# Performance work log

Measured on AMD Instinct MI355X. Metric: run time of the kernel, lower is better.

Reference implementation:

```python
import jax, jax.numpy as jnp
import numpy as np

N_NODES = 50000
N_EDGES = 800000
HIDDEN = 128
BN_EPS = 1e-5
LEAKY_SLOPE = 0.01


def setup_inputs() -> dict:
    key = jax.random.key(0)
    ks = jax.random.split(key, 8)
    x = jax.random.normal(ks[0], (N_NODES, HIDDEN), dtype=jnp.float32)
    edge_index = jax.random.randint(ks[1], (2, N_EDGES), 0, N_NODES, dtype=jnp.int64)
    # stacked per-layer params (4 SAGEConv layers, all 128->128)
    sc = 1.0 / np.sqrt(HIDDEN)
    Wl = jax.random.normal(ks[2], (4, HIDDEN, HIDDEN), dtype=jnp.float32) * sc
    bl = jax.random.normal(ks[3], (4, HIDDEN), dtype=jnp.float32) * sc
    Wr = jax.random.normal(ks[4], (4, HIDDEN, HIDDEN), dtype=jnp.float32) * sc
    gamma = jnp.ones((4, HIDDEN), dtype=jnp.float32)
    beta = jnp.zeros((4, HIDDEN), dtype=jnp.float32)
    return {"x": x, "edge_index": edge_index, "Wl": Wl, "bl": bl,
            "Wr": Wr, "gamma": gamma, "beta": beta}


def _sage_mean_agg(x, src, dst, n):
    # gather source features per edge, scatter-mean onto destination nodes
    msg = x[src]                                                  # [E, F]
    agg = jax.ops.segment_sum(msg, dst, num_segments=n)           # [N, F]
    cnt = jax.ops.segment_sum(jnp.ones_like(dst, dtype=x.dtype), dst, num_segments=n)
    return agg / jnp.maximum(cnt, 1.0)[:, None]


def _bn_train(x, g, b):
    mu = jnp.mean(x, axis=0)
    var = jnp.mean((x - mu) ** 2, axis=0)  # biased variance (PyTorch BN normalization)
    return (x - mu) * jax.lax.rsqrt(var + BN_EPS) * g + b


def reference(x, edge_index, Wl, bl, Wr, gamma, beta):
    src, dst = edge_index[0], edge_index[1]
    n = x.shape[0]
    h = x
    for i in range(4):
        agg = _sage_mean_agg(h, src, dst, n)
        h = agg @ Wl[i] + bl[i] + h @ Wr[i]          # SAGEConv: lin_l(mean_nbr) + lin_r(root)
        h = jnp.where(h >= 0, h, LEAKY_SLOPE * h)    # leaky_relu
        h = _bn_train(h, gamma[i], beta[i])
    # dropout: eval-mode identity (deterministic reference)
    return h
```

## Files before the change

kernel.cpp:

```cpp
#include <hip/hip_runtime.h>
#include <hip/hip_bf16.h>

#define N_NODES 50000
#define N_EDGES 800000
#define F 128
#define BN_EPS 1e-5f
#define SLOPE 0.01f
#define NB 782
#define CAP 64
#define NGRP 8
#define GSZ (N_NODES / NGRP)
#define QCAP 131072
#define ABLK 128
#define AITER ((N_EDGES + ABLK * 256 - 1) / (ABLK * 256))
#define SBLK 512

typedef __attribute__((ext_vector_type(8))) __bf16 bf16x8_t;
typedef __attribute__((ext_vector_type(8))) unsigned short u16x8_t;
typedef __attribute__((ext_vector_type(4))) float f32x4_t;

__device__ __forceinline__ unsigned short f2b(float f) {
    unsigned int u = __float_as_uint(f);
    unsigned int r = (u + 0x7fffu + ((u >> 16) & 1u)) >> 16;
    return (unsigned short)r;
}
__device__ __forceinline__ float b2f_lo(unsigned int v) { return __uint_as_float(v << 16); }
__device__ __forceinline__ float b2f_hi(unsigned int v) { return __uint_as_float(v & 0xffff0000u); }

__global__ __launch_bounds__(256) void bucket_kernel(const int* __restrict__ src,
                                                     const int* __restrict__ dst,
                                                     int* __restrict__ qtail,
                                                     unsigned int* __restrict__ qdata) {
    __shared__ unsigned int bins[4][NGRP][128];
    const int tid = threadIdx.x;
    const int lane = tid & 63;
    const int w = tid >> 6;
    int bc[NGRP];
#pragma unroll
    for (int k = 0; k < NGRP; ++k) bc[k] = 0;

    const int stride = ABLK * 256;
    for (int it = 0; it < AITER; ++it) {
        const int e = blockIdx.x * 256 + tid + it * stride;
        const bool valid = e < N_EDGES;
        int g = -1;
        unsigned int pack = 0;
        if (valid) {
            int d = __builtin_nontemporal_load(dst + e);
            int s = __builtin_nontemporal_load(src + e);
            g = d / GSZ;
            pack = ((unsigned int)d << 16) | (unsigned int)s;
        }
#pragma unroll
        for (int k = 0; k < NGRP; ++k) {
            unsigned long long mask = __ballot(g == k);
            int cnt = __popcll(mask);
            if (!cnt) continue;
            int cur = bc[k];
            if (cur + cnt > 128) {
                int qb = 0;
                if (lane == 0) qb = atomicAdd(&qtail[k * 16], cur);
                qb = __shfl(qb, 0);
                for (int j = lane; j < cur; j += 64)
                    qdata[(long)k * QCAP + qb + j] = bins[w][k][j];
                cur = 0;
            }
            if (g == k) {
                int rank = __popcll(mask & ((1ull << lane) - 1ull));
                bins[w][k][cur + rank] = pack;
            }
            bc[k] = cur + cnt;
        }
    }
#pragma unroll
    for (int k = 0; k < NGRP; ++k) {
        int cur = bc[k];
        if (cur) {
            int qb = 0;
            if (lane == 0) qb = atomicAdd(&qtail[k * 16], cur);
            qb = __shfl(qb, 0);
            for (int j = lane; j < cur; j += 64)
                qdata[(long)k * QCAP + qb + j] = bins[w][k][j];
        }
    }
}

__global__ void scatter_kernel(const unsigned int* __restrict__ qdata,
                               const int* __restrict__ qtail,
                               int* __restrict__ deg_pad,
                               unsigned short* __restrict__ csr) {
    const int g = blockIdx.x & 7;
    const int bg = blockIdx.x >> 3;
    const int n = qtail[g * 16];
    const unsigned int* q = qdata + (long)g * QCAP;
    for (int i = bg * 256 + threadIdx.x; i < n; i += (SBLK / 8) * 256) {
        unsigned int p = __builtin_nontemporal_load(q + i);
        int d = p >> 16;
        int s = p & 0xffff;
        int pos = atomicAdd(&deg_pad[d * 16], 1);
        if (pos < CAP) csr[d * CAP + pos] = (unsigned short)s;
    }
}


__global__ __launch_bounds__(256) void f2b_kernel(const float* __restrict__ in,
                                                  unsigned short* __restrict__ out) {
    long i = (long)blockIdx.x * blockDim.x + threadIdx.x;
    if (i >= (long)N_NODES * (F / 4)) return;
    float4 v = ((const float4*)in)[i];
    ushort4 o;
    o.x = f2b(v.x); o.y = f2b(v.y); o.z = f2b(v.z); o.w = f2b(v.w);
    ((ushort4*)out)[i] = o;
}

__global__ __launch_bounds__(256) void wprep_kernel(const float* __restrict__ Wl,
                                                    const float* __restrict__ Wr,
                                                    unsigned short* __restrict__ Wt) {
    int idx = blockIdx.x * blockDim.x + threadIdx.x;
    if (idx >= 4 * F * 256) return;
    int k = idx & 255;
    int n = (idx >> 8) & 127;
    int i = idx >> 15;
    float v = (k < F) ? Wl[((long)i * F + k) * F + n] : Wr[((long)i * F + (k - F)) * F + n];
    Wt[idx] = f2b(v);
}

__global__ void ident_kernel(float* __restrict__ scale, float* __restrict__ shift) {
    int j = threadIdx.x;
    if (j < F) { scale[j] = 1.f; shift[j] = 0.f; }
}


__global__ __launch_bounds__(256) void agg_kernel(const unsigned short* __restrict__ h,
                                                  const int* __restrict__ deg_pad,
                                                  const unsigned short* __restrict__ csr,
                                                  const float* __restrict__ scale,
                                                  const float* __restrict__ shift,
                                                  unsigned short* __restrict__ agg) {
    int node = (int)((blockIdx.x * (unsigned)blockDim.x + threadIdx.x) >> 6);
    int lane = threadIdx.x & 63;
    if (node >= N_NODES) return;
    const int d = deg_pad[node * 16];
    const int beg = node * CAP;
    const int end = beg + d;
    const unsigned short* hl = h + lane * 2;
    float ax = 0.f, ay = 0.f;
    for (int e = beg; e < end; e += 16) {
        int idx[16];
#pragma unroll
        for (int j = 0; j < 16; ++j) {
            int ee = e + j;
            idx[j] = (int)csr[(ee < end) ? ee : beg];
        }
        unsigned int v[16];
#pragma unroll
        for (int j = 0; j < 16; ++j)
            v[j] = *(const unsigned int*)(hl + (long)idx[j] * F);
#pragma unroll
        for (int j = 0; j < 16; ++j) {
            unsigned int m = (e + j < end) ? v[j] : 0u;
            ax += b2f_lo(m);
            ay += b2f_hi(m);
        }
    }
    if (d > 0) {
        const float inv = 1.0f / (float)d;
        const float2 sc = ((const float2*)scale)[lane];
        const float2 sh = ((const float2*)shift)[lane];
        ax = ax * inv * sc.x + sh.x;
        ay = ay * inv * sc.y + sh.y;
    } else {
        ax = 0.f; ay = 0.f;
    }
    unsigned int o = (unsigned int)f2b(ax) | ((unsigned int)f2b(ay) << 16);
    *(unsigned int*)(agg + (long)node * F + lane * 2) = o;
}

__device__ __forceinline__ u16x8_t affine8(u16x8_t av, const float* __restrict__ sc,
                                           const float* __restrict__ sh) {
    u16x8_t r;
#pragma unroll
    for (int j = 0; j < 8; ++j) {
        float v = __uint_as_float(((unsigned int)av[j]) << 16);
        v = v * sc[j] + sh[j];
        r[j] = f2b(v);
    }
    return r;
}

__global__ __launch_bounds__(256) void gemm_mfma(const unsigned short* __restrict__ aggb,
                                                 const unsigned short* __restrict__ hin,
                                                 const float* __restrict__ scale,
                                                 const float* __restrict__ shift,
                                                 const unsigned short* __restrict__ Wt,
                                                 const float* __restrict__ bl,
                                                 float* __restrict__ Pf,
                                                 unsigned short* __restrict__ Pb,
                                                 int write_bf16,
                                                 float* __restrict__ partial) {
    __shared__ __align__(16) char shraw[64 * 136 * 4];
    unsigned short* stage = (unsigned short*)shraw;
    unsigned short* ep16 = (unsigned short*)shraw;
    float* ep32 = (float*)shraw;
    __shared__ float lsum[4][F];
    __shared__ float lsq[4][F];

    const int tid = threadIdx.x;
    const int wave = tid >> 6, lane = tid & 63;
    const int m = lane & 15, q = lane >> 4;
    const int rbase = blockIdx.x * 64 + wave * 16;
    const int arow = rbase + m;
    const bool aval = arow < N_NODES;
    const unsigned short* ap = aggb + (long)arow * F + q * 8;
    const unsigned short* hp = hin + (long)arow * F + q * 8;

    u16x8_t areg[8];
#pragma unroll
    for (int j = 0; j < 8; ++j) areg[j] = (u16x8_t)0;
    if (aval) {
#pragma unroll
        for (int j = 0; j < 4; ++j) areg[j] = *(const u16x8_t*)(ap + j * 32);
#pragma unroll
        for (int j = 0; j < 4; ++j) {
            u16x8_t raw = *(const u16x8_t*)(hp + j * 32);
            const int base = j * 32 + q * 8;
            areg[4 + j] = affine8(raw, scale + base, shift + base);
        }
    }

    f32x4_t acc[8];
#pragma unroll
    for (int nt = 0; nt < 8; ++nt) acc[nt] = (f32x4_t){0.f, 0.f, 0.f, 0.f};

    for (int half = 0; half < 2; ++half) {
        if (half) __syncthreads();
#pragma unroll
        for (int f = 0; f < 8; ++f) {
            const int fid = f * 256 + tid;
            const int lf = fid & 63;
            const int ksf = (fid >> 6) & 3;
            const int ntf = fid >> 8;
            const int n = ntf * 16 + (lf & 15);
            const int k = half * 128 + ksf * 32 + (lf >> 4) * 8;
            *(u16x8_t*)(stage + fid * 8) = *(const u16x8_t*)(Wt + (long)n * 256 + k);
        }
        __syncthreads();
#pragma unroll
        for (int ks = 0; ks < 4; ++ks) {
            bf16x8_t af = __builtin_bit_cast(bf16x8_t, areg[half * 4 + ks]);
#pragma unroll
            for (int nt = 0; nt < 8; ++nt) {
                u16x8_t bv = *(const u16x8_t*)(stage + ((nt * 4 + ks) * 64 + lane) * 8);
                bf16x8_t bf = __builtin_bit_cast(bf16x8_t, bv);
                acc[nt] = __builtin_amdgcn_mfma_f32_16x16x32_bf16(af, bf, acc[nt], 0, 0, 0);
            }
        }
    }

    __syncthreads();

    float cs[8], cq[8];
#pragma unroll
    for (int nt = 0; nt < 8; ++nt) {
        cs[nt] = 0.f; cq[nt] = 0.f;
        const int c = nt * 16 + m;
        const float b = bl[c];
#pragma unroll
        for (int r = 0; r < 4; ++r) {
            const int rl = wave * 16 + q * 4 + r;
            float v = acc[nt][r] + b;
            v = (v >= 0.f) ? v : SLOPE * v;
            if (write_bf16) ep16[rl * 136 + c] = f2b(v);
            else            ep32[rl * 136 + c] = v;
            if (rbase + q * 4 + r < N_NODES) {
                cs[nt] += v;
                cq[nt] += v * v;
            }
        }
    }

    {
        const int rq = lane >> 4;
        const int cc = (lane & 15) * 8;
#pragma unroll
        for (int r2 = 0; r2 < 4; ++r2) {
            const int rl = wave * 16 + rq * 4 + r2;
            const int grow = blockIdx.x * 64 + rl;
            if (grow < N_NODES) {
                if (write_bf16) {
                    *(u16x8_t*)(Pb + (long)grow * F + cc) =
                        *(const u16x8_t*)(ep16 + rl * 136 + cc);
                } else {
                    *(f32x4_t*)(Pf + (long)grow * F + cc) =
                        *(const f32x4_t*)(ep32 + rl * 136 + cc);
                    *(f32x4_t*)(Pf + (long)grow * F + cc + 4) =
                        *(const f32x4_t*)(ep32 + rl * 136 + cc + 4);
                }
            }
        }
    }

#pragma unroll
    for (int nt = 0; nt < 8; ++nt) {
        cs[nt] += __shfl_xor(cs[nt], 16);
        cs[nt] += __shfl_xor(cs[nt], 32);
        cq[nt] += __shfl_xor(cq[nt], 16);
        cq[nt] += __shfl_xor(cq[nt], 32);
    }
    if (lane < 16) {
#pragma unroll
        for (int nt = 0; nt < 8; ++nt) {
            lsum[wave][nt * 16 + m] = cs[nt];
            lsq[wave][nt * 16 + m] = cq[nt];
        }
    }
    __syncthreads();
    if (tid < F) {
        float s = 0.f, s2 = 0.f;
#pragma unroll
        for (int w = 0; w < 4; ++w) {
            s += lsum[w][tid];
            s2 += lsq[w][tid];
        }
        partial[(long)blockIdx.x * 256 + tid] = s;
        partial[(long)blockIdx.x * 256 + 128 + tid] = s2;
    }
}

__global__ __launch_bounds__(256) void bn_reduce(const float* __restrict__ partial,
                                                 const float* __restrict__ gamma,
                                                 const float* __restrict__ beta,
                                                 float* __restrict__ scale,
                                                 float* __restrict__ shift) {
    const int j = blockIdx.x;
    const int t = threadIdx.x;
    const int lane = t & 63, wave = t >> 6;
    float s = 0.f, s2 = 0.f;
    for (int b = t; b < NB; b += 256) {
        s += partial[(long)b * 256 + j];
        s2 += partial[(long)b * 256 + 128 + j];
    }
#pragma unroll
    for (int off = 1; off < 64; off <<= 1) {
        s += __shfl_xor(s, off);
        s2 += __shfl_xor(s2, off);
    }
    __shared__ float ls[4], lq[4];
    if (lane == 0) { ls[wave] = s; lq[wave] = s2; }
    __syncthreads();
    if (t == 0) {
        float S = ls[0] + ls[1] + ls[2] + ls[3];
        float Q = lq[0] + lq[1] + lq[2] + lq[3];
        const float inv_n = 1.0f / (float)N_NODES;
        float mu = S * inv_n;
        float var = Q * inv_n - mu * mu;
        float scl = gamma[j] * rsqrtf(var + BN_EPS);
        scale[j] = scl;
        shift[j] = beta[j] - mu * scl;
    }
}

__global__ __launch_bounds__(256) void bn_apply_f(float* __restrict__ P,
                                                  const float* __restrict__ scale,
                                                  const float* __restrict__ shift) {
    long i = (long)blockIdx.x * blockDim.x + threadIdx.x;
    if (i >= (long)N_NODES * (F / 4)) return;
    const int c4 = (int)(i & 31);
    float4 v = ((float4*)P)[i];
    const float4 sc = ((const float4*)scale)[c4];
    const float4 sh = ((const float4*)shift)[c4];
    v.x = v.x * sc.x + sh.x;
    v.y = v.y * sc.y + sh.y;
    v.z = v.z * sc.z + sh.z;
    v.w = v.w * sc.w + sh.w;
    ((float4*)P)[i] = v;
}


extern "C" void kernel_launch(void* const* d_in, const int* in_sizes, int n_in,
                              void* d_out, int out_size, void* d_ws, size_t ws_size,
                              hipStream_t stream) {
    const float* x     = (const float*)d_in[0];
    const int*   ei    = (const int*)d_in[1];
    const float* Wl    = (const float*)d_in[2];
    const float* bl    = (const float*)d_in[3];
    const float* Wr    = (const float*)d_in[4];
    const float* gamma = (const float*)d_in[5];
    const float* beta  = (const float*)d_in[6];
    float* out = (float*)d_out;

    const int* src = ei;
    const int* dst = ei + N_EDGES;

    char* w = (char*)d_ws;
    auto alloc = [&](size_t bytes) -> char* {
        char* p = w;
        w += (bytes + 255) & ~(size_t)255;
        return p;
    };
    unsigned short* hbA   = (unsigned short*)alloc((size_t)N_NODES * F * 2);
    unsigned short* hbB   = (unsigned short*)alloc((size_t)N_NODES * F * 2);
    unsigned short* aggb  = (unsigned short*)alloc((size_t)N_NODES * F * 2);
    unsigned short* Wt    = (unsigned short*)alloc((size_t)4 * F * 256 * 2);
    int*   deg_pad  = (int*)alloc((size_t)N_NODES * 16 * 4);
    int*   qtail    = (int*)alloc(8 * 16 * 4);
    unsigned int* qdata = (unsigned int*)alloc((size_t)NGRP * QCAP * 4);
    unsigned short* csr = (unsigned short*)alloc((size_t)N_NODES * CAP * 2);
    float* partial  = (float*)alloc((size_t)NB * 256 * 4);
    float* scale    = (float*)alloc(F * 4);
    float* shift    = (float*)alloc(F * 4);

    hipMemsetAsync(deg_pad, 0, (size_t)N_NODES * 16 * 4 + 8 * 16 * 4, stream);

    bucket_kernel<<<ABLK, 256, 0, stream>>>(src, dst, qtail, qdata);
    scatter_kernel<<<SBLK, 256, 0, stream>>>(qdata, qtail, deg_pad, csr);

    const int n4 = N_NODES * (F / 4);
    f2b_kernel<<<(n4 + 255) / 256, 256, 0, stream>>>(x, hbA);
    wprep_kernel<<<(4 * F * 256 + 255) / 256, 256, 0, stream>>>(Wl, Wr, Wt);
    ident_kernel<<<1, 128, 0, stream>>>(scale, shift);

    unsigned short* hin = hbA;
    unsigned short* hnext = hbB;
    for (int i = 0; i < 4; ++i) {
        const int last = (i == 3);

        agg_kernel<<<(N_NODES + 3) / 4, 256, 0, stream>>>(hin, deg_pad, csr, scale, shift, aggb);

        gemm_mfma<<<NB, 256, 0, stream>>>(
            aggb, hin, scale, shift, Wt + (size_t)i * F * 256, bl + (size_t)i * F,
            out, hnext, last ? 0 : 1, partial);

        bn_reduce<<<F, 256, 0, stream>>>(partial, gamma + (size_t)i * F, beta + (size_t)i * F,
                                         scale, shift);

        unsigned short* t = hin; hin = hnext; hnext = t;
    }
    bn_apply_f<<<(n4 + 255) / 256, 256, 0, stream>>>(out, scale, shift);
}
```

Measured before the change: 416.5 us.

## Build CSR per node range in LDS and store degrees densely

The scatter kernel now gives each block a fixed range of 98 destination nodes within a group. Each block scans that group's entire queue, counts and stages neighbor indices in shared memory with LDS atomics, then writes CSR rows with vectorized coalesced stores and a dense degree array. This removes global atomics on the padded degree array and shrinks the memset to only the queue tails. The bucket kernel block count is also raised. The cost is that every block re-reads the full group queue, which multiplies L2 read traffic by the number of blocks per group.

```diff
diff --git a/kernel.cpp b/kernel.cpp
--- a/kernel.cpp
+++ b/kernel.cpp
@@ -11,9 +11,9 @@
 #define NGRP 8
 #define GSZ (N_NODES / NGRP)
 #define QCAP 131072
-#define ABLK 128
+#define ABLK 512
 #define AITER ((N_EDGES + ABLK * 256 - 1) / (ABLK * 256))
-#define SBLK 512
+#define SUB 98
 
 typedef __attribute__((ext_vector_type(8))) __bf16 bf16x8_t;
 typedef __attribute__((ext_vector_type(8))) unsigned short u16x8_t;
@@ -85,21 +85,39 @@
     }
 }
 
-__global__ void scatter_kernel(const unsigned int* __restrict__ qdata,
-                               const int* __restrict__ qtail,
-                               int* __restrict__ deg_pad,
-                               unsigned short* __restrict__ csr) {
+__global__ __launch_bounds__(256) void scatter_kernel(const unsigned int* __restrict__ qdata,
+                                                      const int* __restrict__ qtail,
+                                                      int* __restrict__ deg,
+                                                      unsigned short* __restrict__ csr) {
+    __shared__ int counts[SUB];
+    __shared__ unsigned short stage[SUB][CAP];
     const int g = blockIdx.x & 7;
     const int bg = blockIdx.x >> 3;
+    const int base = g * GSZ + bg * SUB;
+    const int nn = min(SUB, g * GSZ + GSZ - base);
+    const int tid = threadIdx.x;
+
+    for (int r = tid; r < SUB; r += 256) counts[r] = 0;
+    __syncthreads();
+
     const int n = qtail[g * 16];
     const unsigned int* q = qdata + (long)g * QCAP;
-    for (int i = bg * 256 + threadIdx.x; i < n; i += (SBLK / 8) * 256) {
+    for (int i = tid; i < n; i += 256) {
         unsigned int p = __builtin_nontemporal_load(q + i);
-        int d = p >> 16;
-        int s = p & 0xffff;
-        int pos = atomicAdd(&deg_pad[d * 16], 1);
-        if (pos < CAP) csr[d * CAP + pos] = (unsigned short)s;
-    }
+        int local = (int)(p >> 16) - base;
+        if (local >= 0 && local < nn) {
+            int pos = atomicAdd(&counts[local], 1);
+            if (pos < CAP) stage[local][pos] = (unsigned short)(p & 0xffff);
+        }
+    }
+    __syncthreads();
+
+    for (int c = tid; c < nn * (CAP / 8); c += 256) {
+        const int r = c >> 3;
+        const int col = (c & 7) * 8;
+        *(u16x8_t*)(csr + (long)(base + r) * CAP + col) = *(const u16x8_t*)&stage[r][col];
+    }
+    for (int r = tid; r < nn; r += 256) deg[base + r] = min(counts[r], CAP);
 }
 
 
@@ -132,7 +150,7 @@
 
 
 __global__ __launch_bounds__(256) void agg_kernel(const unsigned short* __restrict__ h,
-                                                  const int* __restrict__ deg_pad,
+                                                  const int* __restrict__ deg,
                                                   const unsigned short* __restrict__ csr,
                                                   const float* __restrict__ scale,
                                                   const float* __restrict__ shift,
@@ -140,7 +158,7 @@
     int node = (int)((blockIdx.x * (unsigned)blockDim.x + threadIdx.x) >> 6);
     int lane = threadIdx.x & 63;
     if (node >= N_NODES) return;
-    const int d = deg_pad[node * 16];
+    const int d = deg[node];
     const int beg = node * CAP;
     const int end = beg + d;
     const unsigned short* hl = h + lane * 2;
@@ -402,7 +420,7 @@
     unsigned short* hbB   = (unsigned short*)alloc((size_t)N_NODES * F * 2);
     unsigned short* aggb  = (unsigned short*)alloc((size_t)N_NODES * F * 2);
     unsigned short* Wt    = (unsigned short*)alloc((size_t)4 * F * 256 * 2);
-    int*   deg_pad  = (int*)alloc((size_t)N_NODES * 16 * 4);
+    int*   deg      = (int*)alloc((size_t)N_NODES * 4);
     int*   qtail    = (int*)alloc(8 * 16 * 4);
     unsigned int* qdata = (unsigned int*)alloc((size_t)NGRP * QCAP * 4);
     unsigned short* csr = (unsigned short*)alloc((size_t)N_NODES * CAP * 2);
@@ -410,10 +428,10 @@
     float* scale    = (float*)alloc(F * 4);
     float* shift    = (float*)alloc(F * 4);
 
-    hipMemsetAsync(deg_pad, 0, (size_t)N_NODES * 16 * 4 + 8 * 16 * 4, stream);
+    hipMemsetAsync(qtail, 0, 8 * 16 * 4, stream);
 
     bucket_kernel<<<ABLK, 256, 0, stream>>>(src, dst, qtail, qdata);
-    scatter_kernel<<<SBLK, 256, 0, stream>>>(qdata, qtail, deg_pad, csr);
+    scatter_kernel<<<512, 256, 0, stream>>>(qdata, qtail, deg, csr);
 
     const int n4 = N_NODES * (F / 4);
     f2b_kernel<<<(n4 + 255) / 256, 256, 0, stream>>>(x, hbA);
@@ -425,7 +443,7 @@
     for (int i = 0; i < 4; ++i) {
         const int last = (i == 3);
 
-        agg_kernel<<<(N_NODES + 3) / 4, 256, 0, stream>>>(hin, deg_pad, csr, scale, shift, aggb);
+        agg_kernel<<<(N_NODES + 3) / 4, 256, 0, stream>>>(hin, deg, csr, scale, shift, aggb);
 
         gemm_mfma<<<NB, 256, 0, stream>>>(
             aggb, hin, scale, shift, Wt + (size_t)i * F * 256, bl + (size_t)i * F,
```

New measurement: 549.4 us. 31.9% more time.
